# Kernel tuning notes

Hardware: AMD Instinct MI355X
Metric: run time of the kernel (lower is better)

## Reference

```python
import jax, jax.numpy as jnp
import numpy as np

EMBED = 512
HEADS = 8
EPS = 1e-5


def setup_inputs() -> dict:
    key = jax.random.key(0)
    ks = jax.random.split(key, 8)
    B, Sq, Skv, D = 4, 2048, 2048, EMBED
    return {
        "layer_input": jax.random.normal(ks[0], (B, Sq, D), jnp.float32),
        "cross_attn_input": jax.random.normal(ks[1], (B, Skv, D), jnp.float32),
        "Wq": jax.random.normal(ks[2], (D, D), jnp.float32) * (D ** -0.5),
        "bq": jnp.zeros((D,), jnp.float32),
        "Wkv": jax.random.normal(ks[3], (D, 2 * D), jnp.float32) * (D ** -0.5),
        "bkv": jnp.zeros((2 * D,), jnp.float32),
        "Wo": jax.random.normal(ks[4], (D, D), jnp.float32) * (D ** -0.5),
        "bo": jnp.zeros((D,), jnp.float32),
        "gamma": jnp.ones((D,), jnp.float32),
        "beta": jnp.zeros((D,), jnp.float32),
    }


def _split_heads(x):
    # ... s (h d) -> ... h s d
    *lead, s, hd = x.shape
    d = hd // HEADS
    return jnp.moveaxis(x.reshape(*lead, s, HEADS, d), -2, -3)


def _merge_heads(x):
    # ... h s d -> ... s (h d)
    x = jnp.moveaxis(x, -3, -2)
    *lead, s, h, d = x.shape
    return x.reshape(*lead, s, h * d)


def reference(layer_input, cross_attn_input, Wq, bq, Wkv, bkv, Wo, bo, gamma, beta):
    scale = (EMBED // HEADS) ** -0.5
    res = layer_input
    q = layer_input @ Wq + bq
    kv = cross_attn_input @ Wkv + bkv
    k, v = jnp.split(kv, 2, axis=-1)
    q, k, v = map(_split_heads, (q, k, v))  # [B, H, S, d]
    scores = jnp.einsum('bhqc,bhkc->bhqk', q, k) * scale
    weights = jax.nn.softmax(scores, axis=-1)  # dropout p=0 -> identity
    out = jnp.einsum('bhqk,bhkc->bhqc', weights, v)
    out = _merge_heads(out)
    out = out @ Wo + bo
    x = out + res
    mu = jnp.mean(x, axis=-1, keepdims=True)
    var = jnp.mean(jnp.square(x - mu), axis=-1, keepdims=True)
    return (x - mu) * jax.lax.rsqrt(var + EPS) * gamma + beta
```

## Files before the change

### kernel.cpp

```cpp
#include <hip/hip_runtime.h>
#include <hip/hip_bf16.h>
#include <stdint.h>

#define SEQ    2048
#define DM     512
#define NHEAD  8
#define HD     64
#define BATCH  4
#define MTOT   (BATCH*SEQ)

typedef __attribute__((ext_vector_type(4))) float  f32x4;
typedef __attribute__((ext_vector_type(8))) short  bf16x8;
typedef __attribute__((ext_vector_type(8))) unsigned short u16x8;
typedef __attribute__((ext_vector_type(4))) unsigned short u16x4;
typedef __attribute__((ext_vector_type(4))) float  fl4;
typedef __attribute__((ext_vector_type(2))) unsigned u32x2;
typedef __attribute__((ext_vector_type(4))) unsigned u32x4;

__device__ __forceinline__ unsigned short f2bf(float f) {
  union { float f; unsigned u; } c; c.f = f;
  return (unsigned short)((c.u + 0x7fffu + ((c.u >> 16) & 1u)) >> 16);
}

__device__ __forceinline__ float bf2f(unsigned short s) {
  unsigned u = (unsigned)s << 16;
  float f; __builtin_memcpy(&f, &u, 4);
  return f;
}

__device__ __forceinline__ void load_lds16(const void* g, void* l) {
  __builtin_amdgcn_global_load_lds((__attribute__((address_space(1))) void*)g,
                                   (__attribute__((address_space(3))) void*)l,
                                   16, 0, 0);
}

__device__ __forceinline__ unsigned pack_bf2(float lo, float hi) {
  __hip_bfloat162 h2 = __float22bfloat162_rn(float2{lo, hi});
  unsigned u; __builtin_memcpy(&u, &h2, 4);
  return u;
}

__global__ void k_pre(const float* __restrict__ X, unsigned short* __restrict__ Xb,
                      const float* __restrict__ C, unsigned short* __restrict__ Cb,
                      const float* __restrict__ Wq, unsigned short* __restrict__ Wqt,
                      const float* __restrict__ Wkv, unsigned short* __restrict__ Wkvt,
                      const float* __restrict__ Wo, unsigned short* __restrict__ Wot) {
  __shared__ __align__(16) unsigned short t[64][66];
  int bid = blockIdx.x, tid = threadIdx.x;
  if (bid < 8192) {
    const float* src = (bid < 4096) ? X : C;
    unsigned short* dst = (bid < 4096) ? Xb : Cb;
    int i = (bid & 4095) * 256 + tid;
    fl4 v = *(const fl4*)(src + (size_t)i * 4);
    u32x2 o;
    o[0] = pack_bf2(v[0], v[1]);
    o[1] = pack_bf2(v[2], v[3]);
    *(u32x2*)((void*)(dst + (size_t)i * 4)) = o;
    return;
  }
  int tjob = bid - 8192;
  const float* W; unsigned short* Wt; int Nd, bx, by;
  if (tjob < 64)       { W = Wq;  Wt = Wqt;  Nd = 512;  bx = tjob & 7;  by = tjob >> 3; }
  else if (tjob < 192) { int u = tjob - 64;  W = Wkv; Wt = Wkvt; Nd = 1024; bx = u & 15; by = u >> 4; }
  else                 { int u = tjob - 192; W = Wo;  Wt = Wot;  Nd = 512;  bx = u & 7;  by = u >> 3; }
  int k0 = by * 64, n0 = bx * 64;
  int r = tid >> 2, cs = (tid & 3) * 16;
  const float* src = W + (size_t)(k0 + r) * Nd + n0 + cs;
#pragma unroll
  for (int i = 0; i < 4; ++i) {
    fl4 v = *(const fl4*)(src + i * 4);
    *(unsigned*)&t[r][cs + i*4]     = pack_bf2(v[0], v[1]);
    *(unsigned*)&t[r][cs + i*4 + 2] = pack_bf2(v[2], v[3]);
  }
  __syncthreads();
  unsigned short* drow = Wt + (size_t)(n0 + r) * 512 + k0 + cs;
#pragma unroll
  for (int half = 0; half < 2; ++half) {
    u16x8 o;
#pragma unroll
    for (int i = 0; i < 8; ++i) o[i] = t[cs + half*8 + i][r];
    *(u16x8*)(drow + half * 8) = o;
  }
}

template<int MODE>
__device__ __forceinline__ void gemm128x64(
    const unsigned short* __restrict__ A,
    const unsigned short* __restrict__ Bt,
    const float* __restrict__ bias,
    const unsigned short* __restrict__ res,
    unsigned short* __restrict__ Cout,
    int N, int K, int m0, int n0, float osc,
    unsigned short* Als, unsigned short* Bls,
    unsigned short* Vt = nullptr, int bh = 0) {
  int tid  = threadIdx.x;
  int lane = tid & 63, wave = tid >> 6;
  int q = lane & 15, lk = lane >> 4;
  f32x4 acc[2][4];
#pragma unroll
  for (int mt = 0; mt < 2; ++mt)
#pragma unroll
    for (int nt = 0; nt < 4; ++nt) acc[mt][nt] = f32x4{0.f,0.f,0.f,0.f};

  const unsigned short* gA[4];
#pragma unroll
  for (int it = 0; it < 4; ++it) {
    int idx = tid + it * 256;
    int row = idx >> 3, ch = idx & 7, sc = ch ^ (row & 7);
    gA[it] = A + (size_t)(m0 + row) * K + sc * 8;
  }
  const unsigned short* gB[2];
#pragma unroll
  for (int it = 0; it < 2; ++it) {
    int idx = tid + it * 256;
    int row = idx >> 3, ch = idx & 7, sc = ch ^ (row & 7);
    gB[it] = Bt + (size_t)(n0 + row) * K + sc * 8;
  }
  char* aD = (char*)Als + tid * 16;
  char* bD = (char*)Bls + tid * 16;

#pragma unroll
  for (int it = 0; it < 4; ++it) { load_lds16(gA[it], aD + it * 4096); gA[it] += 64; }
#pragma unroll
  for (int it = 0; it < 2; ++it) { load_lds16(gB[it], bD + it * 4096); gB[it] += 64; }
  __syncthreads();

  int nkb = K >> 6;
  int buf = 0;
  for (int kb = 0; kb < nkb; ++kb) {
    if (kb + 1 < nkb) {
      char* aN = aD + (buf ^ 1) * 16384;
      char* bN = bD + (buf ^ 1) * 8192;
#pragma unroll
      for (int it = 0; it < 4; ++it) { load_lds16(gA[it], aN + it * 4096); gA[it] += 64; }
#pragma unroll
      for (int it = 0; it < 2; ++it) { load_lds16(gB[it], bN + it * 4096); gB[it] += 64; }
    }
    const char* aR = (const char*)Als + buf * 16384;
    const char* bR = (const char*)Bls + buf * 8192;
#pragma unroll
    for (int ks = 0; ks < 2; ++ks) {
      bf16x8 a[2], b[4];
#pragma unroll
      for (int mt = 0; mt < 2; ++mt) {
        int row = wave * 32 + mt * 16 + q;
        a[mt] = *(const bf16x8*)(aR + row * 128 + (((ks*4 + lk) ^ (row & 7)) * 16));
      }
#pragma unroll
      for (int nt = 0; nt < 4; ++nt) {
        int row = nt * 16 + q;
        b[nt] = *(const bf16x8*)(bR + row * 128 + (((ks*4 + lk) ^ (row & 7)) * 16));
      }
#pragma unroll
      for (int mt = 0; mt < 2; ++mt)
#pragma unroll
        for (int nt = 0; nt < 4; ++nt)
          acc[mt][nt] = __builtin_amdgcn_mfma_f32_16x16x32_bf16(a[mt], b[nt], acc[mt][nt], 0, 0, 0);
    }
    __syncthreads();
    buf ^= 1;
  }
  if (MODE == 2) {
    unsigned short* T = Als;
#pragma unroll
    for (int nt = 0; nt < 4; ++nt) {
      int coll = nt * 16 + q;
      float bv = bias[n0 + coll];
#pragma unroll
      for (int mt = 0; mt < 2; ++mt) {
        int rowl = wave * 32 + mt * 16 + lk * 4;
#pragma unroll
        for (int rr = 0; rr < 4; ++rr)
          T[coll * 136 + rowl + rr] = f2bf(acc[mt][nt][rr] + bv);
      }
    }
    __syncthreads();
    int dv = tid >> 2, c = tid & 3;
    const unsigned short* s = T + dv * 136 + c * 32;
    unsigned short* d = Vt + ((size_t)bh * 64 + dv) * 2048 + (m0 & 2047) + c * 32;
#pragma unroll
    for (int i = 0; i < 4; ++i)
      *(u16x8*)(d + i * 8) = *(const u16x8*)(s + i * 8);
    return;
  }
#pragma unroll
  for (int nt = 0; nt < 4; ++nt) {
    int col = n0 + nt * 16 + q;
    float bv = bias[col];
#pragma unroll
    for (int mt = 0; mt < 2; ++mt) {
      int rowb = m0 + wave * 32 + mt * 16 + lk * 4;
#pragma unroll
      for (int rr = 0; rr < 4; ++rr) {
        float v = acc[mt][nt][rr] + bv;
        size_t off = (size_t)(rowb + rr) * N + col;
        if (MODE == 1) Cout[off] = f2bf(v + bf2f(res[off]));
        else           Cout[off] = f2bf(v * osc);
      }
    }
  }
}

__global__ __launch_bounds__(256, 3)
void k_projmm(const unsigned short* __restrict__ Xb, const unsigned short* __restrict__ Cb,
              const unsigned short* __restrict__ Wqt, const unsigned short* __restrict__ Wkvt,
              const float* __restrict__ bq, const float* __restrict__ bkv,
              unsigned short* __restrict__ Qb, unsigned short* __restrict__ KVb,
              unsigned short* __restrict__ Vt) {
  __shared__ __align__(16) unsigned short Als[2 * 128 * 64];
  __shared__ __align__(16) unsigned short Bls[2 * 64 * 64];
  int bid = blockIdx.x;
  int l = (bid & 7) * 192 + (bid >> 3);
  const float c1 = 0.125f * 1.44269504088896340736f;
  if (l < 512) {
    int m = l >> 3, n = l & 7;
    gemm128x64<0>(Xb, Wqt, bq, nullptr, Qb, 512, 512, m * 128, n * 64, c1, Als, Bls);
  } else {
    int l2 = l - 512;
    int m = l2 >> 4, n = l2 & 15;
    if (n < 8)
      gemm128x64<0>(Cb, Wkvt, bkv, nullptr, KVb, 1024, 512, m * 128, n * 64, 1.0f, Als, Bls);
    else
      gemm128x64<2>(Cb, Wkvt, bkv, nullptr, KVb, 1024, 512, m * 128, n * 64, 1.0f, Als, Bls,
                    Vt, (m >> 4) * 8 + (n - 8));
  }
}

__global__ __launch_bounds__(256, 3)
void k_omm(const unsigned short* __restrict__ Abuf, const unsigned short* __restrict__ Wot,
           const float* __restrict__ bo, const unsigned short* __restrict__ residb,
           unsigned short* __restrict__ tmp) {
  __shared__ __align__(16) unsigned short Als[2 * 128 * 64];
  __shared__ __align__(16) unsigned short Bls[2 * 64 * 64];
  int bid = blockIdx.x;
  int l = (bid & 7) * 64 + (bid >> 3);
  int m = l >> 3, n = l & 7;
  gemm128x64<1>(Abuf, Wot, bo, residb, tmp, 512, 512, m * 128, n * 64, 1.0f, Als, Bls);
}

__global__ __launch_bounds__(256, 2)
void k_attn(const unsigned short* __restrict__ Qb,
            const unsigned short* __restrict__ KVb,
            const unsigned short* __restrict__ Vtg,
            unsigned short* __restrict__ Ab) {
  __shared__ __align__(16) unsigned short Klds[2][4096];
  __shared__ __align__(16) unsigned short Vlds[3][4096];
  int tid  = threadIdx.x;
  int lane = tid & 63;
  int q    = lane & 15, lk = lane >> 4;
  int bid = blockIdx.x;
  int swz = (bid & 7) * 64 + (bid >> 3);
  int qt = swz & 15, bh = swz >> 4;
  int b  = bh >> 3, h = bh & 7;
  int q0 = qt * 128 + (tid >> 6) * 32;
  const size_t kvbase = (size_t)b * SEQ * 1024;

  bf16x8 qf[2][2];
#pragma unroll
  for (int qh = 0; qh < 2; ++qh) {
    size_t qrow = (size_t)b * SEQ + q0 + qh * 16 + q;
    qf[qh][0] = *(const bf16x8*)(Qb + qrow * DM + h * HD + lk * 8);
    qf[qh][1] = *(const bf16x8*)(Qb + qrow * DM + h * HD + 32 + lk * 8);
  }
  f32x4 acc[2][4];
#pragma unroll
  for (int qh = 0; qh < 2; ++qh)
#pragma unroll
    for (int i = 0; i < 4; ++i) acc[qh][i] = f32x4{0.f,0.f,0.f,0.f};
  float l0 = 0.f, l1 = 0.f;
  u32x4 pbA[2][2];

  const unsigned short *gK0, *gK1, *gV0, *gV1;
  {
    int r0 = tid >> 3, s0_ = (tid & 7) ^ (r0 & 7);
    gK0 = KVb + kvbase + (size_t)r0 * 1024 + h * HD + s0_ * 8;
    int i1 = tid + 256, r1 = i1 >> 3, s1_ = (i1 & 7) ^ (r1 & 7);
    gK1 = KVb + kvbase + (size_t)r1 * 1024 + h * HD + s1_ * 8;
    gV0 = Vtg + ((size_t)bh * 64 + r0) * 2048 + s0_ * 8;
    gV1 = Vtg + ((size_t)bh * 64 + r1) * 2048 + s1_ * 8;
  }
  char* kw0 = (char*)Klds[0] + tid * 16;
  char* kw1 = (char*)Klds[1] + tid * 16;
  char* vw0 = (char*)Vlds[0] + tid * 16;
  char* vw1 = (char*)Vlds[1] + tid * 16;
  char* vw2 = (char*)Vlds[2] + tid * 16;
  const char* kr0 = (const char*)Klds[0];
  const char* kr1 = (const char*)Klds[1];
  const char* vr0 = (const char*)Vlds[0];
  const char* vr1 = (const char*)Vlds[1];
  const char* vr2 = (const char*)Vlds[2];

#define STAGE(kd_, vd_) do {                        \
    load_lds16(gK0, (kd_));                         \
    load_lds16(gK1, (kd_) + 4096);                  \
    load_lds16(gV0, (vd_));                         \
    load_lds16(gV1, (vd_) + 4096);                  \
    gK0 += 65536; gK1 += 65536;                     \
    gV0 += 64; gV1 += 64;                           \
  } while (0)

#define ABODY(DO_PV, DO_STAGE, kdst_, vdst_, krd_, vprd_) do {               \
    if (DO_STAGE) STAGE(kdst_, vdst_);                                       \
    if (DO_PV) {                                                             \
      bf16x8 vf0[4], vf1[4];                                                 \
      _Pragma("unroll")                                                      \
      for (int dt = 0; dt < 4; ++dt) {                                       \
        int row = dt * 16 + q;                                               \
        vf0[dt] = *(const bf16x8*)((vprd_) + row * 128 + ((lk ^ (q & 7)) * 16)); \
        vf1[dt] = *(const bf16x8*)((vprd_) + row * 128 + (((4 + lk) ^ (q & 7)) * 16)); \
      }                                                                      \
      __builtin_amdgcn_s_setprio(1);                                         \
      {                                                                      \
        union { u32x4 u; bf16x8 v; } pb;                                     \
        _Pragma("unroll")                                                    \
        for (int qh = 0; qh < 2; ++qh) {                                     \
          pb.u = pbA[qh][0];                                                 \
          _Pragma("unroll")                                                  \
          for (int dt = 0; dt < 4; ++dt)                                     \
            acc[qh][dt] = __builtin_amdgcn_mfma_f32_16x16x32_bf16(vf0[dt], pb.v, acc[qh][dt], 0, 0, 0); \
          pb.u = pbA[qh][1];                                                 \
          _Pragma("unroll")                                                  \
          for (int dt = 0; dt < 4; ++dt)                                     \
            acc[qh][dt] = __builtin_amdgcn_mfma_f32_16x16x32_bf16(vf1[dt], pb.v, acc[qh][dt], 0, 0, 0); \
        }                                                                    \
      }                                                                      \
      __builtin_amdgcn_s_setprio(0);                                         \
    }                                                                        \
    f32x4 st[2][4];                                                          \
    _Pragma("unroll")                                                        \
    for (int qh = 0; qh < 2; ++qh)                                           \
      _Pragma("unroll")                                                      \
      for (int kt = 0; kt < 4; ++kt) st[qh][kt] = f32x4{0.f,0.f,0.f,0.f};    \
    __builtin_amdgcn_s_setprio(1);                                           \
    _Pragma("unroll")                                                        \
    for (int kt = 0; kt < 4; ++kt) {                                         \
      int row = kt * 16 + q;                                                 \
      bf16x8 kf0 = *(const bf16x8*)((krd_) + row * 128 + ((lk ^ (q & 7)) * 16)); \
      bf16x8 kf1 = *(const bf16x8*)((krd_) + row * 128 + (((4 + lk) ^ (q & 7)) * 16)); \
      st[0][kt] = __builtin_amdgcn_mfma_f32_16x16x32_bf16(kf0, qf[0][0], st[0][kt], 0, 0, 0); \
      st[0][kt] = __builtin_amdgcn_mfma_f32_16x16x32_bf16(kf1, qf[0][1], st[0][kt], 0, 0, 0); \
      st[1][kt] = __builtin_amdgcn_mfma_f32_16x16x32_bf16(kf0, qf[1][0], st[1][kt], 0, 0, 0); \
      st[1][kt] = __builtin_amdgcn_mfma_f32_16x16x32_bf16(kf1, qf[1][1], st[1][kt], 0, 0, 0); \
    }                                                                        \
    __builtin_amdgcn_s_setprio(0);                                           \
    _Pragma("unroll")                                                        \
    for (int qh = 0; qh < 2; ++qh) {                                         \
      float p[4][4];                                                         \
      _Pragma("unroll")                                                      \
      for (int kt = 0; kt < 4; ++kt)                                         \
        _Pragma("unroll")                                                    \
        for (int r = 0; r < 4; ++r) {                                        \
          float pe = __builtin_amdgcn_exp2f(st[qh][kt][r]);                  \
          p[kt][r] = pe;                                                     \
          if (qh) l1 += pe; else l0 += pe;                                   \
        }                                                                    \
      _Pragma("unroll")                                                      \
      for (int ks2 = 0; ks2 < 2; ++ks2) {                                    \
        unsigned u0 = pack_bf2(p[2*ks2][0],     p[2*ks2][1]);                \
        unsigned u1 = pack_bf2(p[2*ks2][2],     p[2*ks2][3]);                \
        unsigned u2 = pack_bf2(p[2*ks2 + 1][0], p[2*ks2 + 1][1]);            \
        unsigned u3 = pack_bf2(p[2*ks2 + 1][2], p[2*ks2 + 1][3]);            \
        asm("v_permlane32_swap_b32 %0, %1" : "+v"(u0), "+v"(u2));            \
        asm("v_permlane32_swap_b32 %0, %1" : "+v"(u1), "+v"(u3));            \
        asm("v_permlane16_swap_b32 %0, %1" : "+v"(u0), "+v"(u2));            \
        asm("v_permlane16_swap_b32 %0, %1" : "+v"(u1), "+v"(u3));            \
        pbA[qh][ks2][0] = u0; pbA[qh][ks2][1] = u1;                          \
        pbA[qh][ks2][2] = u2; pbA[qh][ks2][3] = u3;                          \
      }                                                                      \
    }                                                                        \
    __syncthreads();                                                         \
  } while (0)

  STAGE(kw0, vw0);
  __syncthreads();

  ABODY(0, 1, kw1, vw1, kr0, vr0);
  for (int g = 0; g < 5; ++g) {
    ABODY(1, 1, kw0, vw2, kr1, vr0);
    ABODY(1, 1, kw1, vw0, kr0, vr1);
    ABODY(1, 1, kw0, vw1, kr1, vr2);
    ABODY(1, 1, kw1, vw2, kr0, vr0);
    ABODY(1, 1, kw0, vw0, kr1, vr1);
    ABODY(1, 1, kw1, vw1, kr0, vr2);
  }
  ABODY(1, 0, kw0, vw0, kr1, vr0);

  {
    bf16x8 vf0[4], vf1[4];
#pragma unroll
    for (int dt = 0; dt < 4; ++dt) {
      int row = dt * 16 + q;
      vf0[dt] = *(const bf16x8*)(vr1 + row * 128 + ((lk ^ (q & 7)) * 16));
      vf1[dt] = *(const bf16x8*)(vr1 + row * 128 + (((4 + lk) ^ (q & 7)) * 16));
    }
    union { u32x4 u; bf16x8 v; } pb;
#pragma unroll
    for (int qh = 0; qh < 2; ++qh) {
      pb.u = pbA[qh][0];
#pragma unroll
      for (int dt = 0; dt < 4; ++dt)
        acc[qh][dt] = __builtin_amdgcn_mfma_f32_16x16x32_bf16(vf0[dt], pb.v, acc[qh][dt], 0, 0, 0);
      pb.u = pbA[qh][1];
#pragma unroll
      for (int dt = 0; dt < 4; ++dt)
        acc[qh][dt] = __builtin_amdgcn_mfma_f32_16x16x32_bf16(vf1[dt], pb.v, acc[qh][dt], 0, 0, 0);
    }
  }

#pragma unroll
  for (int qh = 0; qh < 2; ++qh) {
    float lv = qh ? l1 : l0;
    lv += __shfl_xor(lv, 16);
    lv += __shfl_xor(lv, 32);
    float inv = 1.0f / lv;
    size_t orow = ((size_t)b * SEQ + q0 + qh * 16 + q) * DM + h * HD + lk * 4;
#pragma unroll
    for (int dt = 0; dt < 4; ++dt) {
      u16x4 o;
#pragma unroll
      for (int r = 0; r < 4; ++r) o[r] = f2bf(acc[qh][dt][r] * inv);
      *(u16x4*)(Ab + orow + dt * 16) = o;
    }
  }
#undef STAGE
#undef ABODY
}

__global__ void k_ln(const unsigned short* __restrict__ x, const float* __restrict__ gamma,
                     const float* __restrict__ beta, float* __restrict__ out) {
  int tid = threadIdx.x, lane = tid & 63, wave = tid >> 6;
  size_t row = (size_t)blockIdx.x * 4 + wave;
  u16x8 xv = *(const u16x8*)(x + row * DM + lane * 8);
  float v[8];
#pragma unroll
  for (int i = 0; i < 8; ++i) v[i] = bf2f(xv[i]);
  float s  = (v[0]+v[1]) + (v[2]+v[3]) + (v[4]+v[5]) + (v[6]+v[7]);
  float ss = (v[0]*v[0]+v[1]*v[1]) + (v[2]*v[2]+v[3]*v[3])
           + (v[4]*v[4]+v[5]*v[5]) + (v[6]*v[6]+v[7]*v[7]);
#pragma unroll
  for (int off = 1; off < 64; off <<= 1) {
    s  += __shfl_xor(s, off);
    ss += __shfl_xor(ss, off);
  }
  float mu  = s * (1.0f / DM);
  float var = ss * (1.0f / DM) - mu * mu;
  float w = rsqrtf(var + 1e-5f);
  fl4 g0 = *(const fl4*)(gamma + lane*8), g1 = *(const fl4*)(gamma + lane*8 + 4);
  fl4 b0 = *(const fl4*)(beta + lane*8),  b1 = *(const fl4*)(beta + lane*8 + 4);
  fl4 o0, o1;
#pragma unroll
  for (int i = 0; i < 4; ++i) {
    o0[i] = (v[i]     - mu) * w * g0[i] + b0[i];
    o1[i] = (v[4 + i] - mu) * w * g1[i] + b1[i];
  }
  float* orow = out + row * DM + lane * 8;
  *(fl4*)orow = o0;
  *(fl4*)(orow + 4) = o1;
}

extern "C" void kernel_launch(void* const* d_in, const int* in_sizes, int n_in,
                              void* d_out, int out_size, void* d_ws, size_t ws_size,
                              hipStream_t stream) {
  const float* layer_input = (const float*)d_in[0];
  const float* cross       = (const float*)d_in[1];
  const float* Wq   = (const float*)d_in[2];
  const float* bq   = (const float*)d_in[3];
  const float* Wkv  = (const float*)d_in[4];
  const float* bkv  = (const float*)d_in[5];
  const float* Wo   = (const float*)d_in[6];
  const float* bo   = (const float*)d_in[7];
  const float* gamma = (const float*)d_in[8];
  const float* beta  = (const float*)d_in[9];
  float* out = (float*)d_out;

  char* ws = (char*)d_ws;
  unsigned short* Xb   = (unsigned short*)(ws + (size_t)0);
  unsigned short* Cb   = (unsigned short*)(ws + ((size_t)8  << 20));
  unsigned short* Qb   = (unsigned short*)(ws + ((size_t)16 << 20));
  unsigned short* KVb  = (unsigned short*)(ws + ((size_t)24 << 20));
  unsigned short* Abuf = (unsigned short*)(ws + ((size_t)40 << 20));
  unsigned short* Vt   = (unsigned short*)(ws + ((size_t)48 << 20));
  unsigned short* tmpb = (unsigned short*)(ws + ((size_t)48 << 20));
  unsigned short* Wqt  = (unsigned short*)(ws + ((size_t)64 << 20));
  unsigned short* Wkvt = (unsigned short*)(ws + ((size_t)65 << 20));
  unsigned short* Wot  = (unsigned short*)(ws + ((size_t)67 << 20));

  k_pre<<<8448, 256, 0, stream>>>(layer_input, Xb, cross, Cb,
                                  Wq, Wqt, Wkv, Wkvt, Wo, Wot);
  k_projmm<<<1536, 256, 0, stream>>>(Xb, Cb, Wqt, Wkvt, bq, bkv, Qb, KVb, Vt);
  k_attn<<<512, 256, 0, stream>>>(Qb, KVb, Vt, Abuf);
  k_omm<<<512, 256, 0, stream>>>(Abuf, Wot, bo, Xb, tmpb);
  k_ln<<<MTOT/4, 256, 0, stream>>>(tmpb, gamma, beta, out);
}
```

Baseline: 99.97 us.

## Split attention KV sequence across two wave groups per block and merge partials

The attention kernel now launches 512 threads per block, in two groups of 256. Each group processes half of the 2048-key sequence using its own K/V LDS buffers, so the per-group loop is unrolled to 16 steps instead of 32. The partial accumulators and row sums from group 1 are passed through shared memory and added into group 0 before normalisation and store. This raises wave-level parallelism for the fixed 512-block grid at the cost of doubled LDS, an extra reduction step, and fewer active threads during the epilogue. The merge adds the two partials without any max rescaling, which matches the before code's softmax handling.

```diff
diff --git a/kernel.cpp b/kernel.cpp
--- a/kernel.cpp
+++ b/kernel.cpp
@@ -238,21 +238,23 @@
   gemm128x64<1>(Abuf, Wot, bo, residb, tmp, 512, 512, m * 128, n * 64, 1.0f, Als, Bls);
 }
 
-__global__ __launch_bounds__(256, 2)
+__global__ __launch_bounds__(512, 2)
 void k_attn(const unsigned short* __restrict__ Qb,
             const unsigned short* __restrict__ KVb,
             const unsigned short* __restrict__ Vtg,
             unsigned short* __restrict__ Ab) {
-  __shared__ __align__(16) unsigned short Klds[2][4096];
-  __shared__ __align__(16) unsigned short Vlds[3][4096];
+  __shared__ __align__(16) unsigned short Klds[2][2][4096];
+  __shared__ __align__(16) unsigned short Vlds[2][3][4096];
   int tid  = threadIdx.x;
+  int ltid = tid & 255;
+  int grp  = tid >> 8;
   int lane = tid & 63;
   int q    = lane & 15, lk = lane >> 4;
   int bid = blockIdx.x;
   int swz = (bid & 7) * 64 + (bid >> 3);
   int qt = swz & 15, bh = swz >> 4;
   int b  = bh >> 3, h = bh & 7;
-  int q0 = qt * 128 + (tid >> 6) * 32;
+  int q0 = qt * 128 + ((ltid >> 6)) * 32;
   const size_t kvbase = (size_t)b * SEQ * 1024;
 
   bf16x8 qf[2][2];
@@ -272,23 +274,23 @@
 
   const unsigned short *gK0, *gK1, *gV0, *gV1;
   {
-    int r0 = tid >> 3, s0_ = (tid & 7) ^ (r0 & 7);
-    gK0 = KVb + kvbase + (size_t)r0 * 1024 + h * HD + s0_ * 8;
-    int i1 = tid + 256, r1 = i1 >> 3, s1_ = (i1 & 7) ^ (r1 & 7);
-    gK1 = KVb + kvbase + (size_t)r1 * 1024 + h * HD + s1_ * 8;
-    gV0 = Vtg + ((size_t)bh * 64 + r0) * 2048 + s0_ * 8;
-    gV1 = Vtg + ((size_t)bh * 64 + r1) * 2048 + s1_ * 8;
-  }
-  char* kw0 = (char*)Klds[0] + tid * 16;
-  char* kw1 = (char*)Klds[1] + tid * 16;
-  char* vw0 = (char*)Vlds[0] + tid * 16;
-  char* vw1 = (char*)Vlds[1] + tid * 16;
-  char* vw2 = (char*)Vlds[2] + tid * 16;
-  const char* kr0 = (const char*)Klds[0];
-  const char* kr1 = (const char*)Klds[1];
-  const char* vr0 = (const char*)Vlds[0];
-  const char* vr1 = (const char*)Vlds[1];
-  const char* vr2 = (const char*)Vlds[2];
+    int r0 = ltid >> 3, s0_ = (ltid & 7) ^ (r0 & 7);
+    gK0 = KVb + kvbase + (size_t)grp * 1048576 + (size_t)r0 * 1024 + h * HD + s0_ * 8;
+    int i1 = ltid + 256, r1 = i1 >> 3, s1_ = (i1 & 7) ^ (r1 & 7);
+    gK1 = KVb + kvbase + (size_t)grp * 1048576 + (size_t)r1 * 1024 + h * HD + s1_ * 8;
+    gV0 = Vtg + ((size_t)bh * 64 + r0) * 2048 + grp * 1024 + s0_ * 8;
+    gV1 = Vtg + ((size_t)bh * 64 + r1) * 2048 + grp * 1024 + s1_ * 8;
+  }
+  char* kw0 = (char*)Klds[grp][0] + ltid * 16;
+  char* kw1 = (char*)Klds[grp][1] + ltid * 16;
+  char* vw0 = (char*)Vlds[grp][0] + ltid * 16;
+  char* vw1 = (char*)Vlds[grp][1] + ltid * 16;
+  char* vw2 = (char*)Vlds[grp][2] + ltid * 16;
+  const char* kr0 = (const char*)Klds[grp][0];
+  const char* kr1 = (const char*)Klds[grp][1];
+  const char* vr0 = (const char*)Vlds[grp][0];
+  const char* vr1 = (const char*)Vlds[grp][1];
+  const char* vr2 = (const char*)Vlds[grp][2];
 
 #define STAGE(kd_, vd_) do {                        \
     load_lds16(gK0, (kd_));                         \
@@ -375,23 +377,29 @@
   __syncthreads();
 
   ABODY(0, 1, kw1, vw1, kr0, vr0);
-  for (int g = 0; g < 5; ++g) {
-    ABODY(1, 1, kw0, vw2, kr1, vr0);
-    ABODY(1, 1, kw1, vw0, kr0, vr1);
-    ABODY(1, 1, kw0, vw1, kr1, vr2);
-    ABODY(1, 1, kw1, vw2, kr0, vr0);
-    ABODY(1, 1, kw0, vw0, kr1, vr1);
-    ABODY(1, 1, kw1, vw1, kr0, vr2);
-  }
-  ABODY(1, 0, kw0, vw0, kr1, vr0);
+  ABODY(1, 1, kw0, vw2, kr1, vr0);
+  ABODY(1, 1, kw1, vw0, kr0, vr1);
+  ABODY(1, 1, kw0, vw1, kr1, vr2);
+  ABODY(1, 1, kw1, vw2, kr0, vr0);
+  ABODY(1, 1, kw0, vw0, kr1, vr1);
+  ABODY(1, 1, kw1, vw1, kr0, vr2);
+  ABODY(1, 1, kw0, vw2, kr1, vr0);
+  ABODY(1, 1, kw1, vw0, kr0, vr1);
+  ABODY(1, 1, kw0, vw1, kr1, vr2);
+  ABODY(1, 1, kw1, vw2, kr0, vr0);
+  ABODY(1, 1, kw0, vw0, kr1, vr1);
+  ABODY(1, 1, kw1, vw1, kr0, vr2);
+  ABODY(1, 1, kw0, vw2, kr1, vr0);
+  ABODY(1, 1, kw1, vw0, kr0, vr1);
+  ABODY(1, 0, kw0, vw0, kr1, vr2);
 
   {
     bf16x8 vf0[4], vf1[4];
 #pragma unroll
     for (int dt = 0; dt < 4; ++dt) {
       int row = dt * 16 + q;
-      vf0[dt] = *(const bf16x8*)(vr1 + row * 128 + ((lk ^ (q & 7)) * 16));
-      vf1[dt] = *(const bf16x8*)(vr1 + row * 128 + (((4 + lk) ^ (q & 7)) * 16));
+      vf0[dt] = *(const bf16x8*)(vr0 + row * 128 + ((lk ^ (q & 7)) * 16));
+      vf1[dt] = *(const bf16x8*)(vr0 + row * 128 + (((4 + lk) ^ (q & 7)) * 16));
     }
     union { u32x4 u; bf16x8 v; } pb;
 #pragma unroll
@@ -407,19 +415,46 @@
     }
   }
 
-#pragma unroll
-  for (int qh = 0; qh < 2; ++qh) {
-    float lv = qh ? l1 : l0;
-    lv += __shfl_xor(lv, 16);
-    lv += __shfl_xor(lv, 32);
-    float inv = 1.0f / lv;
-    size_t orow = ((size_t)b * SEQ + q0 + qh * 16 + q) * DM + h * HD + lk * 4;
-#pragma unroll
-    for (int dt = 0; dt < 4; ++dt) {
-      u16x4 o;
-#pragma unroll
-      for (int r = 0; r < 4; ++r) o[r] = f2bf(acc[qh][dt][r] * inv);
-      *(u16x4*)(Ab + orow + dt * 16) = o;
+  __syncthreads();
+  float* S = (float*)Vlds;
+  if (grp == 1) {
+    int base = ltid * 37;
+#pragma unroll
+    for (int qh = 0; qh < 2; ++qh)
+#pragma unroll
+      for (int dt = 0; dt < 4; ++dt)
+#pragma unroll
+        for (int r = 0; r < 4; ++r)
+          S[base + qh * 16 + dt * 4 + r] = acc[qh][dt][r];
+    S[base + 32] = l0;
+    S[base + 33] = l1;
+  }
+  __syncthreads();
+  if (grp == 0) {
+    int base = ltid * 37;
+#pragma unroll
+    for (int qh = 0; qh < 2; ++qh)
+#pragma unroll
+      for (int dt = 0; dt < 4; ++dt)
+#pragma unroll
+        for (int r = 0; r < 4; ++r)
+          acc[qh][dt][r] += S[base + qh * 16 + dt * 4 + r];
+    l0 += S[base + 32];
+    l1 += S[base + 33];
+#pragma unroll
+    for (int qh = 0; qh < 2; ++qh) {
+      float lv = qh ? l1 : l0;
+      lv += __shfl_xor(lv, 16);
+      lv += __shfl_xor(lv, 32);
+      float inv = 1.0f / lv;
+      size_t orow = ((size_t)b * SEQ + q0 + qh * 16 + q) * DM + h * HD + lk * 4;
+#pragma unroll
+      for (int dt = 0; dt < 4; ++dt) {
+        u16x4 o;
+#pragma unroll
+        for (int r = 0; r < 4; ++r) o[r] = f2bf(acc[qh][dt][r] * inv);
+        *(u16x4*)(Ab + orow + dt * 16) = o;
+      }
     }
   }
 #undef STAGE
@@ -488,7 +523,7 @@
   k_pre<<<8448, 256, 0, stream>>>(layer_input, Xb, cross, Cb,
                                   Wq, Wqt, Wkv, Wkvt, Wo, Wot);
   k_projmm<<<1536, 256, 0, stream>>>(Xb, Cb, Wqt, Wkvt, bq, bkv, Qb, KVb, Vt);
-  k_attn<<<512, 256, 0, stream>>>(Qb, KVb, Vt, Abuf);
+  k_attn<<<512, 512, 0, stream>>>(Qb, KVb, Vt, Abuf);
   k_omm<<<512, 256, 0, stream>>>(Abuf, Wot, bo, Xb, tmpb);
   k_ln<<<MTOT/4, 256, 0, stream>>>(tmpb, gamma, beta, out);
 }
```

Result: slower. 102.8 us (+2.8%).

## Halve attention block size to 64 query rows with 128 threads

Applied to the files above, without the earlier changes.

The attention kernel now uses 128-thread blocks covering 64 query rows each, with twice as many blocks and launch bounds targeting four blocks per CU. The K/V staging is rewritten so each thread issues four 16-byte loads per tile instead of two. This aims at finer-grained scheduling and better load balance across CUs. The cost is that K/V tiles are loaded into LDS twice as often per query row, which raises memory traffic and LDS pressure.

```diff
diff --git a/kernel.cpp b/kernel.cpp
--- a/kernel.cpp
+++ b/kernel.cpp
@@ -238,7 +238,7 @@
   gemm128x64<1>(Abuf, Wot, bo, residb, tmp, 512, 512, m * 128, n * 64, 1.0f, Als, Bls);
 }
 
-__global__ __launch_bounds__(256, 2)
+__global__ __launch_bounds__(128, 4)
 void k_attn(const unsigned short* __restrict__ Qb,
             const unsigned short* __restrict__ KVb,
             const unsigned short* __restrict__ Vtg,
@@ -249,10 +249,10 @@
   int lane = tid & 63;
   int q    = lane & 15, lk = lane >> 4;
   int bid = blockIdx.x;
-  int swz = (bid & 7) * 64 + (bid >> 3);
-  int qt = swz & 15, bh = swz >> 4;
+  int swz = (bid & 7) * 128 + (bid >> 3);
+  int qt = swz & 31, bh = swz >> 5;
   int b  = bh >> 3, h = bh & 7;
-  int q0 = qt * 128 + (tid >> 6) * 32;
+  int q0 = qt * 64 + (tid >> 6) * 32;
   const size_t kvbase = (size_t)b * SEQ * 1024;
 
   bf16x8 qf[2][2];
@@ -270,14 +270,13 @@
   float l0 = 0.f, l1 = 0.f;
   u32x4 pbA[2][2];
 
-  const unsigned short *gK0, *gK1, *gV0, *gV1;
-  {
-    int r0 = tid >> 3, s0_ = (tid & 7) ^ (r0 & 7);
-    gK0 = KVb + kvbase + (size_t)r0 * 1024 + h * HD + s0_ * 8;
-    int i1 = tid + 256, r1 = i1 >> 3, s1_ = (i1 & 7) ^ (r1 & 7);
-    gK1 = KVb + kvbase + (size_t)r1 * 1024 + h * HD + s1_ * 8;
-    gV0 = Vtg + ((size_t)bh * 64 + r0) * 2048 + s0_ * 8;
-    gV1 = Vtg + ((size_t)bh * 64 + r1) * 2048 + s1_ * 8;
+  const unsigned short *gK[4], *gV[4];
+#pragma unroll
+  for (int it = 0; it < 4; ++it) {
+    int idx = tid + it * 128;
+    int r = idx >> 3, sc = (idx & 7) ^ (r & 7);
+    gK[it] = KVb + kvbase + (size_t)r * 1024 + h * HD + sc * 8;
+    gV[it] = Vtg + ((size_t)bh * 64 + r) * 2048 + sc * 8;
   }
   char* kw0 = (char*)Klds[0] + tid * 16;
   char* kw1 = (char*)Klds[1] + tid * 16;
@@ -290,13 +289,17 @@
   const char* vr1 = (const char*)Vlds[1];
   const char* vr2 = (const char*)Vlds[2];
 
-#define STAGE(kd_, vd_) do {                        \
-    load_lds16(gK0, (kd_));                         \
-    load_lds16(gK1, (kd_) + 4096);                  \
-    load_lds16(gV0, (vd_));                         \
-    load_lds16(gV1, (vd_) + 4096);                  \
-    gK0 += 65536; gK1 += 65536;                     \
-    gV0 += 64; gV1 += 64;                           \
+#define STAGE(kd_, vd_) do {                                        \
+    _Pragma("unroll")                                               \
+    for (int it = 0; it < 4; ++it) {                                \
+      load_lds16(gK[it], (kd_) + it * 2048);                        \
+      gK[it] += 65536;                                              \
+    }                                                               \
+    _Pragma("unroll")                                               \
+    for (int it = 0; it < 4; ++it) {                                \
+      load_lds16(gV[it], (vd_) + it * 2048);                        \
+      gV[it] += 64;                                                 \
+    }                                                               \
   } while (0)
 
 #define ABODY(DO_PV, DO_STAGE, kdst_, vdst_, krd_, vprd_) do {               \
@@ -488,7 +491,7 @@
   k_pre<<<8448, 256, 0, stream>>>(layer_input, Xb, cross, Cb,
                                   Wq, Wqt, Wkv, Wkvt, Wo, Wot);
   k_projmm<<<1536, 256, 0, stream>>>(Xb, Cb, Wqt, Wkvt, bq, bkv, Qb, KVb, Vt);
-  k_attn<<<512, 256, 0, stream>>>(Qb, KVb, Vt, Abuf);
+  k_attn<<<1024, 128, 0, stream>>>(Qb, KVb, Vt, Abuf);
   k_omm<<<512, 256, 0, stream>>>(Abuf, Wot, bo, Xb, tmpb);
   k_ln<<<MTOT/4, 256, 0, stream>>>(tmpb, gamma, beta, out);
 }
```

New measurement: 106.6 us. 1.07x slower.
